# Performance work log

Hardware: AMD Instinct MI355X
Metric: run time of the kernel (lower is better)

The kernel has to match this reference:

```python
import jax, jax.numpy as jnp
import numpy as np

B, S, H, KV, D, HID = 1, 2048, 32, 8, 128, 4096
SCALE = D ** -0.5
EPS = 1e-5
QMAX = 127.0  # 8-bit symmetric fake quant


def fake_quant(x):
    # per-tensor symmetric int8 fake quantization with straight-through estimator
    s = jnp.maximum(jnp.max(jnp.abs(x)), 1e-5) / QMAX
    q = jnp.clip(jnp.round(x / s), -QMAX - 1.0, QMAX) * s
    return x + jax.lax.stop_gradient(q - x)


def rms_norm(x, w):
    xf = x.astype(jnp.float32)
    var = jnp.mean(xf * xf, axis=-1, keepdims=True)
    return (xf * jax.lax.rsqrt(var + EPS)).astype(x.dtype) * w


def rotate_half(x):
    h = x.shape[-1] // 2
    return jnp.concatenate([-x[..., h:], x[..., :h]], axis=-1)


def qlinear(x, W):
    # QuantLinear: fake-quant activation and weight, then matmul (no bias)
    return fake_quant(x) @ fake_quant(W).T


def setup_inputs() -> dict:
    key = jax.random.key(0)
    ks = jax.random.split(key, 5)
    hidden_states = jax.random.normal(ks[0], (B, S, HID), jnp.float32)
    # RoPE tables
    inv_freq = 1.0 / (10000.0 ** (np.arange(0, D, 2, dtype=np.float32) / D))
    freqs = np.outer(np.arange(S, dtype=np.float32), inv_freq)  # [S, D/2]
    emb = np.concatenate([freqs, freqs], axis=-1)  # [S, D]
    cos = jnp.asarray(np.cos(emb))[None]  # [1,S,D]
    sin = jnp.asarray(np.sin(emb))[None]
    # causal additive mask [1,1,S,S]
    mask = jnp.where(np.tril(np.ones((S, S), dtype=bool)), 0.0, -1e9).astype(jnp.float32)[None, None]
    Wq = jax.random.normal(ks[1], (H * D, HID), jnp.float32) * 0.02
    Wk = jax.random.normal(ks[2], (KV * D, HID), jnp.float32) * 0.02
    Wv = jax.random.normal(ks[3], (KV * D, HID), jnp.float32) * 0.02
    Wo = jax.random.normal(ks[4], (HID, H * D), jnp.float32) * 0.02
    q_norm_w = jnp.ones((D,), jnp.float32)
    k_norm_w = jnp.ones((D,), jnp.float32)
    return dict(hidden_states=hidden_states, cos=cos, sin=sin, attention_mask=mask,
                Wq=Wq, Wk=Wk, Wv=Wv, Wo=Wo, q_norm_w=q_norm_w, k_norm_w=k_norm_w)


def reference(hidden_states, cos, sin, attention_mask, Wq, Wk, Wv, Wo, q_norm_w, k_norm_w):
    b, s, _ = hidden_states.shape
    q = qlinear(hidden_states, Wq).reshape(b, s, H, D).transpose(0, 2, 1, 3)   # [B,H,S,D]
    k = qlinear(hidden_states, Wk).reshape(b, s, KV, D).transpose(0, 2, 1, 3)  # [B,KV,S,D]
    v = qlinear(hidden_states, Wv).reshape(b, s, KV, D).transpose(0, 2, 1, 3)
    q = rms_norm(q, q_norm_w)
    k = rms_norm(k, k_norm_w)
    c = cos[:, None]  # unsqueeze head dim -> [1,1,S,D]
    sn = sin[:, None]
    q = q * c + rotate_half(q) * sn
    k = k * c + rotate_half(k) * sn
    n_rep = H // KV
    k = jnp.repeat(k, n_rep, axis=1)  # [B,H,S,D]
    v = jnp.repeat(v, n_rep, axis=1)
    # fake-quant around QK^T
    q = fake_quant(q)
    k = fake_quant(k)
    scores = jnp.einsum('bhqd,bhkd->bhqk', q, k) * SCALE + attention_mask
    p = jax.nn.softmax(scores.astype(jnp.float32), axis=-1).astype(q.dtype)
    # fake-quant around PV
    p = fake_quant(p)
    v = fake_quant(v)
    out = jnp.einsum('bhqk,bhkd->bhqd', p, v)
    out = out.transpose(0, 2, 1, 3).reshape(b, s, H * D)
    return qlinear(out, Wo)
```

## Files before the change

kernel.cpp:

```cpp
#include <hip/hip_runtime.h>
#include <hip/hip_bf16.h>
#include <math.h>
#include <stdint.h>

#define S_LEN 2048
#define NH    32
#define NKV   8
#define HD    128
#define HIDD  4096

typedef unsigned short u16;
typedef __attribute__((ext_vector_type(4))) int i32x4;

#define GLD16(g, l) __builtin_amdgcn_global_load_lds( \
    (const __attribute__((address_space(1))) void*)(g), \
    (__attribute__((address_space(3))) void*)(l), 16, 0, 0)


__device__ __forceinline__ float slot_scale(const unsigned* slot) {
    return fmaxf(__uint_as_float(*slot), 1e-5f) / 127.0f;
}

__device__ __forceinline__ float exp2_fast(float x) {
    float r; asm("v_exp_f32 %0, %1" : "=v"(r) : "v"(x)); return r;
}
__device__ __forceinline__ float log2_fast(float x) {
    float r; asm("v_log_f32 %0, %1" : "=v"(r) : "v"(x)); return r;
}

__device__ __forceinline__ int qint(float x, float s) {
    float q = rintf(x / s);
    q = fminf(fmaxf(q, -128.0f), 127.0f);
    return (int)q;
}

__device__ __forceinline__ void block_amax_atomic(float m, unsigned* slot) {
    __shared__ float wmax[8];
    const int lane = threadIdx.x & 63;
    const int wid  = threadIdx.x >> 6;
    const int nw   = blockDim.x >> 6;
    #pragma unroll
    for (int o = 32; o; o >>= 1) m = fmaxf(m, __shfl_xor(m, o));
    if (lane == 0) wmax[wid] = m;
    __syncthreads();
    if (threadIdx.x == 0) {
        float bm = wmax[0];
        for (int i = 1; i < nw; ++i) bm = fmaxf(bm, wmax[i]);
        atomicMax(slot, __float_as_uint(bm));
    }
}

struct Amax5Args { const float* p[5]; size_t n4[5]; };
__global__ __launch_bounds__(256) void absmax5_kernel(Amax5Args a, unsigned* slots) {
    const int t = blockIdx.y;
    const float4* x4 = (const float4*)a.p[t];
    const size_t n4 = a.n4[t];
    size_t i = (size_t)blockIdx.x * blockDim.x + threadIdx.x;
    size_t stride = (size_t)gridDim.x * blockDim.x;
    float m = 0.0f;
    for (; i < n4; i += stride) {
        float4 v = x4[i];
        m = fmaxf(m, fmaxf(fmaxf(fabsf(v.x), fabsf(v.y)), fmaxf(fabsf(v.z), fabsf(v.w))));
    }
    block_amax_atomic(m, slots + t);
}

struct Quant5Args { const float* p[5]; char* o[5]; size_t n4[5]; };
__global__ __launch_bounds__(256) void quant5_kernel(Quant5Args a, const unsigned* slots) {
    const int t = blockIdx.y;
    float s = slot_scale(slots + t);
    const float4* x4 = (const float4*)a.p[t];
    unsigned* o4 = (unsigned*)a.o[t];
    const size_t n4 = a.n4[t];
    size_t i = (size_t)blockIdx.x * blockDim.x + threadIdx.x;
    size_t stride = (size_t)gridDim.x * blockDim.x;
    for (; i < n4; i += stride) {
        float4 v = x4[i];
        unsigned o = (unsigned)(qint(v.x, s) & 255)
                   | ((unsigned)(qint(v.y, s) & 255) << 8)
                   | ((unsigned)(qint(v.z, s) & 255) << 16)
                   | ((unsigned)(qint(v.w, s) & 255) << 24);
        o4[i] = o;
    }
}

__global__ __launch_bounds__(256) void quant_kernel(const float* __restrict__ x,
                                                    size_t n4, const unsigned* slot,
                                                    char* __restrict__ out) {
    float s = slot_scale(slot);
    size_t i = (size_t)blockIdx.x * blockDim.x + threadIdx.x;
    size_t stride = (size_t)gridDim.x * blockDim.x;
    const float4* x4 = (const float4*)x;
    unsigned* o4 = (unsigned*)out;
    for (; i < n4; i += stride) {
        float4 v = x4[i];
        unsigned o = (unsigned)(qint(v.x, s) & 255)
                   | ((unsigned)(qint(v.y, s) & 255) << 8)
                   | ((unsigned)(qint(v.z, s) & 255) << 16)
                   | ((unsigned)(qint(v.w, s) & 255) << 24);
        o4[i] = o;
    }
}

__device__ __forceinline__ void gemm_body(const char* __restrict__ A,
                                          const char* __restrict__ B,
                                          float* __restrict__ C,
                                          int m0, int n0, int N, int K,
                                          float scale,
                                          char* Asm, char* Bsm) {
    const int tid  = threadIdx.x;
    const int lane = tid & 63;
    const int wave = tid >> 6;
    const int wr = (wave >> 1) * 64;
    const int wc = (wave & 1) * 64;
    const int l15 = lane & 15;
    const int l4  = lane >> 4;
    const int cx  = (l4 ^ (l15 & 3)) * 16;
    const int r0  = tid >> 2;
    const int sc  = ((tid & 3) ^ ((tid >> 2) & 3)) * 16;

    i32x4 acc[4][4];
    #pragma unroll
    for (int i = 0; i < 4; ++i)
        #pragma unroll
        for (int j = 0; j < 4; ++j) acc[i][j] = (i32x4){0, 0, 0, 0};

    auto STAGE = [&](int buf, int k0) {
        GLD16(&A[(size_t)(m0 + r0) * K + k0 + sc],      &Asm[buf * 8192 + wave * 1024]);
        GLD16(&A[(size_t)(m0 + 64 + r0) * K + k0 + sc], &Asm[buf * 8192 + 4096 + wave * 1024]);
        GLD16(&B[(size_t)(n0 + r0) * K + k0 + sc],      &Bsm[buf * 8192 + wave * 1024]);
        GLD16(&B[(size_t)(n0 + 64 + r0) * K + k0 + sc], &Bsm[buf * 8192 + 4096 + wave * 1024]);
    };

    const int NT = K >> 6;
    STAGE(0, 0);
    STAGE(1, 64);
    int cur = 0;
    for (int t = 0; t < NT; ++t) {
        if (t + 1 < NT) {
            asm volatile("s_waitcnt vmcnt(4)" ::: "memory");
        } else {
            asm volatile("s_waitcnt vmcnt(0)" ::: "memory");
        }
        __builtin_amdgcn_sched_barrier(0);
        __builtin_amdgcn_s_barrier();
        __builtin_amdgcn_sched_barrier(0);
        if (t + 2 < NT) {
            int nb = cur + 2; if (nb >= 3) nb -= 3;
            STAGE(nb, (t + 2) << 6);
        }
        i32x4 af[4], bfr[4];
        #pragma unroll
        for (int i = 0; i < 4; ++i)
            af[i] = *(const i32x4*)&Asm[cur * 8192 + (wr + i * 16 + l15) * 64 + cx];
        #pragma unroll
        for (int j = 0; j < 4; ++j)
            bfr[j] = *(const i32x4*)&Bsm[cur * 8192 + (wc + j * 16 + l15) * 64 + cx];
        #pragma unroll
        for (int i = 0; i < 4; ++i)
            #pragma unroll
            for (int j = 0; j < 4; ++j)
                acc[i][j] = __builtin_amdgcn_mfma_i32_16x16x64_i8(af[i], bfr[j], acc[i][j], 0, 0, 0);
        cur += 1; if (cur == 3) cur = 0;
    }

    #pragma unroll
    for (int i = 0; i < 4; ++i)
        #pragma unroll
        for (int j = 0; j < 4; ++j)
            #pragma unroll
            for (int r = 0; r < 4; ++r) {
                int row = m0 + wr + i * 16 + l4 * 4 + r;
                int col = n0 + wc + j * 16 + l15;
                C[(size_t)row * N + col] = (float)acc[i][j][r] * scale;
            }
}

__global__ __launch_bounds__(256) void gemm_qkv_kernel(const char* __restrict__ Aq,
                                                       const char* __restrict__ Wqq,
                                                       const char* __restrict__ Wkq,
                                                       const char* __restrict__ Wvq,
                                                       float* __restrict__ qf,
                                                       float* __restrict__ kf,
                                                       float* __restrict__ vf,
                                                       const float* __restrict__ cosb,
                                                       const float* __restrict__ sinb,
                                                       const float* __restrict__ qnw,
                                                       const float* __restrict__ knw,
                                                       unsigned* __restrict__ slots) {
    __shared__ __align__(16) char Asm[3 * 8192];
    __shared__ __align__(16) char Bsm[3 * 8192];
    const int tid  = threadIdx.x;
    const int lane = tid & 63;
    const int wave = tid >> 6;
    const int l15 = lane & 15;
    const int l4  = lane >> 4;
    const int cx  = (l4 ^ (l15 & 3)) * 16;
    const int r0  = tid >> 2;
    const int sc  = ((tid & 3) ^ ((tid >> 2) & 3)) * 16;
    const int wr  = wave * 32;

    int bid = blockIdx.x;
    int swz = (bid & 7) * 96 + (bid >> 3);
    int x = swz & 15, y = swz >> 4;
    const char* B; float* C; int N, nb, kind; const unsigned* sB; const float* w;
    if (y < 32)      { B = Wqq; C = qf; N = NH * HD;  nb = y;      sB = slots + 1; kind = 0; w = qnw; }
    else if (y < 40) { B = Wkq; C = kf; N = NKV * HD; nb = y - 32; sB = slots + 2; kind = 1; w = knw; }
    else             { B = Wvq; C = vf; N = NKV * HD; nb = y - 40; sB = slots + 3; kind = 2; w = nullptr; }
    const float scale = slot_scale(slots + 0) * slot_scale(sB);
    const int m0 = x * 128, n0 = nb * 128;

    i32x4 acc[2][8];
    #pragma unroll
    for (int i = 0; i < 2; ++i)
        #pragma unroll
        for (int j = 0; j < 8; ++j) acc[i][j] = (i32x4){0, 0, 0, 0};

    auto STAGE = [&](int buf, int k0) {
        GLD16(&Aq[(size_t)(m0 + r0) * HIDD + k0 + sc],     &Asm[buf * 8192 + wave * 1024]);
        GLD16(&Aq[(size_t)(m0 + 64 + r0) * HIDD + k0 + sc],&Asm[buf * 8192 + 4096 + wave * 1024]);
        GLD16(&B[(size_t)(n0 + r0) * HIDD + k0 + sc],      &Bsm[buf * 8192 + wave * 1024]);
        GLD16(&B[(size_t)(n0 + 64 + r0) * HIDD + k0 + sc], &Bsm[buf * 8192 + 4096 + wave * 1024]);
    };

    const int NT = HIDD >> 6;
    STAGE(0, 0);
    STAGE(1, 64);
    int cur = 0;
    for (int t = 0; t < NT; ++t) {
        if (t + 1 < NT) {
            asm volatile("s_waitcnt vmcnt(4)" ::: "memory");
        } else {
            asm volatile("s_waitcnt vmcnt(0)" ::: "memory");
        }
        __builtin_amdgcn_sched_barrier(0);
        __builtin_amdgcn_s_barrier();
        __builtin_amdgcn_sched_barrier(0);
        if (t + 2 < NT) {
            int nb3 = cur + 2; if (nb3 >= 3) nb3 -= 3;
            STAGE(nb3, (t + 2) << 6);
        }
        i32x4 af[2], bfr[8];
        #pragma unroll
        for (int i = 0; i < 2; ++i)
            af[i] = *(const i32x4*)&Asm[cur * 8192 + (wr + i * 16 + l15) * 64 + cx];
        #pragma unroll
        for (int j = 0; j < 8; ++j)
            bfr[j] = *(const i32x4*)&Bsm[cur * 8192 + (j * 16 + l15) * 64 + cx];
        #pragma unroll
        for (int i = 0; i < 2; ++i)
            #pragma unroll
            for (int j = 0; j < 8; ++j)
                acc[i][j] = __builtin_amdgcn_mfma_i32_16x16x64_i8(af[i], bfr[j], acc[i][j], 0, 0, 0);
        cur += 1; if (cur == 3) cur = 0;
    }

    float lm = 0.0f;
    if (kind == 2) {
        #pragma unroll
        for (int i = 0; i < 2; ++i)
            #pragma unroll
            for (int r = 0; r < 4; ++r) {
                int row = m0 + wr + i * 16 + l4 * 4 + r;
                #pragma unroll
                for (int j = 0; j < 8; ++j) {
                    float v = (float)acc[i][j][r] * scale;
                    C[(size_t)row * N + n0 + j * 16 + l15] = v;
                    lm = fmaxf(lm, fabsf(v));
                }
            }
        __syncthreads();
        block_amax_atomic(lm, slots + 7);
    } else {
        float wj[8];
        #pragma unroll
        for (int j = 0; j < 8; ++j) wj[j] = w[j * 16 + l15];
        #pragma unroll
        for (int i = 0; i < 2; ++i)
            #pragma unroll
            for (int r = 0; r < 4; ++r) {
                int row = m0 + wr + i * 16 + l4 * 4 + r;
                float v[8];
                float ss = 0.0f;
                #pragma unroll
                for (int j = 0; j < 8; ++j) {
                    v[j] = (float)acc[i][j][r] * scale;
                    ss += v[j] * v[j];
                }
                ss += __shfl_xor(ss, 1);
                ss += __shfl_xor(ss, 2);
                ss += __shfl_xor(ss, 4);
                ss += __shfl_xor(ss, 8);
                float inv = 1.0f / sqrtf(ss * (1.0f / 128.0f) + 1e-5f);
                const float* cr = cosb + (size_t)row * 128;
                const float* sr = sinb + (size_t)row * 128;
                float yv[8];
                #pragma unroll
                for (int j = 0; j < 8; ++j) yv[j] = v[j] * inv * wj[j];
                #pragma unroll
                for (int j = 0; j < 8; ++j) {
                    int col = j * 16 + l15;
                    float o = (j < 4) ? yv[j] * cr[col] - yv[j + 4] * sr[col]
                                      : yv[j] * cr[col] + yv[j - 4] * sr[col];
                    C[(size_t)row * N + n0 + col] = o;
                    lm = fmaxf(lm, fabsf(o));
                }
            }
        __syncthreads();
        block_amax_atomic(lm, slots + (kind == 0 ? 5 : 6));
    }
}

__global__ __launch_bounds__(256) void gemm_o_kernel(const char* __restrict__ A,
                                                     const char* __restrict__ Woq,
                                                     float* __restrict__ C,
                                                     const unsigned* __restrict__ slots) {
    __shared__ __align__(16) char Asm[3 * 8192];
    __shared__ __align__(16) char Bsm[3 * 8192];
    int bid = blockIdx.x;
    int swz = (bid & 7) * 64 + (bid >> 3);
    int x = swz & 15, y = swz >> 4;
    float scale = slot_scale(slots + 8) * slot_scale(slots + 4);
    gemm_body(A, Woq, C, x * 128, y * 128, NH * HD, HIDD, scale, Asm, Bsm);
}

__global__ __launch_bounds__(256) void quant_qkv_kernel(const float* __restrict__ qx,
                                                        const float* __restrict__ kx,
                                                        const float* __restrict__ vx,
                                                        const unsigned* slots,
                                                        char* __restrict__ qq,
                                                        char* __restrict__ kq,
                                                        char* __restrict__ vtq) {
    const int bx = blockIdx.x;
    if (bx < 1024) {
        __shared__ unsigned char t8[64][36];
        const float s = slot_scale(slots + 7);
        const int t   = threadIdx.x;
        const int kvh = bx >> 7;
        const int rem = bx & 127;
        const int d0  = (rem & 3) * 32;
        const int sp0 = (rem >> 2) * 64;
        const int dl = t & 31;
        const int sb = t >> 5;
        #pragma unroll
        for (int j = 0; j < 8; ++j) {
            int spl = sb + j * 8;
            float v = vx[((size_t)(sp0 + spl) * NKV + kvh) * 128 + d0 + dl];
            t8[spl][dl] = (unsigned char)qint(v, s);
        }
        __syncthreads();
        const int dd = t >> 3;
        const int ch = t & 7;
        unsigned lo = 0, hi = 0;
        #pragma unroll
        for (int j = 0; j < 4; ++j) lo |= (unsigned)t8[ch * 8 + j][dd] << (8 * j);
        #pragma unroll
        for (int j = 0; j < 4; ++j) hi |= (unsigned)t8[ch * 8 + 4 + j][dd] << (8 * j);
        *(uint2*)&vtq[((size_t)kvh * 128 + d0 + dd) * S_LEN + sp0 + ch * 8] = make_uint2(lo, hi);
        return;
    }
    int tid = (bx - 1024) * 256 + threadIdx.x;
    const int qtot4 = S_LEN * NH * HD / 4;
    if (tid < qtot4) {
        float s = slot_scale(slots + 5);
        int e = tid * 4;
        int d  = e & 127;
        int h  = (e >> 7) & 31;
        int sp = e >> 12;
        float4 v = *(const float4*)&qx[e];
        uchar4 o;
        o.x = (unsigned char)qint(v.x, s); o.y = (unsigned char)qint(v.y, s);
        o.z = (unsigned char)qint(v.z, s); o.w = (unsigned char)qint(v.w, s);
        *(uchar4*)&qq[((size_t)h * S_LEN + sp) * 128 + d] = o;
    } else {
        tid -= qtot4;
        float s = slot_scale(slots + 6);
        int e = tid * 4;
        int d  = e & 127;
        int h  = (e >> 7) & 7;
        int sp = e >> 10;
        float4 v = *(const float4*)&kx[e];
        uchar4 o;
        o.x = (unsigned char)qint(v.x, s); o.y = (unsigned char)qint(v.y, s);
        o.z = (unsigned char)qint(v.z, s); o.w = (unsigned char)qint(v.w, s);
        *(uchar4*)&kq[((size_t)h * S_LEN + sp) * 128 + d] = o;
    }
}

__global__ __launch_bounds__(512) void attn_kernel(const char* __restrict__ Qq,
                                                   const char* __restrict__ Kq,
                                                   const char* __restrict__ Vt,
                                                   const unsigned* sq_slot,
                                                   const unsigned* sk_slot,
                                                   const unsigned* sv_slot,
                                                   float* __restrict__ O,
                                                   unsigned* amax_slot) {
    __shared__ __align__(16) char Klds[64 * 144];
    __shared__ __align__(16) char Vlds[128 * 80];
    __shared__ __align__(16) char plds[8][16 * 80];

    const int tid  = threadIdx.x;
    const int lane = tid & 63;
    const int wave = tid >> 6;
    const int mw   = wave & 3;
    const int h  = blockIdx.y;
    const int kv = h >> 2;
    const int l15 = lane & 15;
    const int l4  = lane >> 4;
    const size_t kvS = (size_t)kv * S_LEN;

    const int qtS = blockIdx.x;
    const int qtB = 31 - qtS;
    const int my_qt = (wave < 4) ? qtB : qtS;
    const int qr0 = my_qt * 64 + mw * 16;

    const float sq = slot_scale(sq_slot);
    const float sk = slot_scale(sk_slot);
    const float sv = slot_scale(sv_slot);
    const float qs2 = sq * sk * 0.08838834764831845f * 1.4426950408889634f;
    const float osc = (1.0f / 127.0f) * sv;
    const float NEG = -1e30f;

    const int krow = tid >> 3, kcol = (tid & 7) * 16;
    const int vrow = tid >> 2, vcol = (tid & 3) * 16;

    i32x4 qf2[2];
    {
        const char* qp = Qq + ((size_t)h * S_LEN + qr0 + l15) * 128 + l4 * 16;
        qf2[0] = *(const i32x4*)(qp);
        qf2[1] = *(const i32x4*)(qp + 64);
    }

    auto qk_block = [&](int hb) -> i32x4 {
        i32x4 sacc = {0, 0, 0, 0};
        #pragma unroll
        for (int c = 0; c < 2; ++c) {
            i32x4 kfa = *(const i32x4*)&Klds[(hb * 16 + l15) * 144 + c * 64 + l4 * 16];
            sacc = __builtin_amdgcn_mfma_i32_16x16x64_i8(kfa, qf2[c], sacc, 0, 0, 0);
        }
        return sacc;
    };

    float m_l = NEG, l_l = 0.0f;

    auto p1_interior = [&](int hb) {
        i32x4 sacc = qk_block(hb);
        float x0 = (float)sacc[0] * qs2, x1 = (float)sacc[1] * qs2;
        float x2 = (float)sacc[2] * qs2, x3 = (float)sacc[3] * qs2;
        float bm = fmaxf(fmaxf(x0, x1), fmaxf(x2, x3));
        float mn = fmaxf(m_l, bm);
        float ps = exp2_fast(x0 - mn) + exp2_fast(x1 - mn)
                 + exp2_fast(x2 - mn) + exp2_fast(x3 - mn);
        l_l = l_l * exp2_fast(m_l - mn) + ps;
        m_l = mn;
    };
    auto p1_diag = [&](int hb) {
        i32x4 sacc = qk_block(hb);
        float x[4];
        #pragma unroll
        for (int r = 0; r < 4; ++r) {
            float v = (float)sacc[r] * qs2;
            x[r] = ((l4 * 4 + r) > l15) ? NEG : v;
        }
        float bm = fmaxf(fmaxf(x[0], x[1]), fmaxf(x[2], x[3]));
        float mn = fmaxf(m_l, bm);
        float ps = exp2_fast(x[0] - mn) + exp2_fast(x[1] - mn)
                 + exp2_fast(x[2] - mn) + exp2_fast(x[3] - mn);
        l_l = l_l * exp2_fast(m_l - mn) + ps;
        m_l = mn;
    };

    i32x4 kreg = *(const i32x4*)&Kq[(kvS + krow) * 128 + kcol];
    #pragma unroll 1
    for (int kc = 0; kc <= qtB; ++kc) {
        __syncthreads();
        *(i32x4*)&Klds[krow * 144 + kcol] = kreg;
        __syncthreads();
        if (kc < qtB)
            kreg = *(const i32x4*)&Kq[(kvS + (kc + 1) * 64 + krow) * 128 + kcol];
        if (kc < my_qt) {
            p1_interior(0); p1_interior(1); p1_interior(2); p1_interior(3);
        } else if (kc == my_qt) {
            #pragma unroll
            for (int hb = 0; hb < 4; ++hb) {
                if (hb < mw) p1_interior(hb);
                else if (hb == mw) p1_diag(hb);
            }
        }
    }
    float cmy;
    {
        float m2 = fmaxf(m_l, __shfl_xor(m_l, 16));
        float mfin = fmaxf(m2, __shfl_xor(m2, 32));
        float t = l_l * exp2_fast(m_l - mfin);
        t += __shfl_xor(t, 16);
        t += __shfl_xor(t, 32);
        cmy = mfin - log2_fast(127.0f / t);
    }

    i32x4 oacc[8];
    #pragma unroll
    for (int dt = 0; dt < 8; ++dt) oacc[dt] = (i32x4){0, 0, 0, 0};

    auto p2_interior = [&](int hb) -> unsigned {
        i32x4 sacc = qk_block(hb);
        unsigned pack = 0;
        #pragma unroll
        for (int r = 0; r < 4; ++r) {
            float pq = rintf(exp2_fast(fmaf((float)sacc[r], qs2, -cmy)));
            pack |= ((unsigned)(int)pq) << (8 * r);
        }
        return pack;
    };
    auto p2_diag = [&](int hb) -> unsigned {
        i32x4 sacc = qk_block(hb);
        unsigned pack = 0;
        #pragma unroll
        for (int r = 0; r < 4; ++r) {
            float p = exp2_fast(fmaf((float)sacc[r], qs2, -cmy));
            float pq = ((l4 * 4 + r) > l15) ? 0.0f : rintf(p);
            pack |= ((unsigned)(int)pq) << (8 * r);
        }
        return pack;
    };
    auto pv8 = [&]() {
        i32x4 pf = *(const i32x4*)&plds[wave][l15 * 80 + l4 * 16];
        __builtin_amdgcn_s_setprio(1);
        #pragma unroll
        for (int dt = 0; dt < 8; ++dt) {
            i32x4 vfb = *(const i32x4*)&Vlds[(dt * 16 + l15) * 80 + l4 * 16];
            oacc[dt] = __builtin_amdgcn_mfma_i32_16x16x64_i8(pf, vfb, oacc[dt], 0, 0, 0);
        }
        __builtin_amdgcn_s_setprio(0);
    };

    kreg = *(const i32x4*)&Kq[(kvS + krow) * 128 + kcol];
    i32x4 vreg = *(const i32x4*)&Vt[((size_t)kv * 128 + vrow) * S_LEN + vcol];
    #pragma unroll 1
    for (int kc = 0; kc <= qtB; ++kc) {
        __syncthreads();
        *(i32x4*)&Klds[krow * 144 + kcol] = kreg;
        *(i32x4*)&Vlds[vrow * 80 + vcol] = vreg;
        __syncthreads();
        if (kc < qtB) {
            kreg = *(const i32x4*)&Kq[(kvS + (kc + 1) * 64 + krow) * 128 + kcol];
            vreg = *(const i32x4*)&Vt[((size_t)kv * 128 + vrow) * S_LEN + (kc + 1) * 64 + vcol];
        }
        if (kc < my_qt) {
            #pragma unroll
            for (int hb = 0; hb < 4; ++hb)
                *(unsigned*)&plds[wave][l15 * 80 + hb * 16 + l4 * 4] = p2_interior(hb);
            pv8();
        } else if (kc == my_qt) {
            #pragma unroll
            for (int hb = 0; hb < 4; ++hb) {
                unsigned pack = 0;
                if (hb < mw) pack = p2_interior(hb);
                else if (hb == mw) pack = p2_diag(hb);
                *(unsigned*)&plds[wave][l15 * 80 + hb * 16 + l4 * 4] = pack;
            }
            pv8();
        }
    }

    float lm = 0.0f;
    #pragma unroll
    for (int dt = 0; dt < 8; ++dt)
        #pragma unroll
        for (int r = 0; r < 4; ++r) {
            float v = (float)oacc[dt][r] * osc;
            O[(size_t)(qr0 + l4 * 4 + r) * (NH * 128) + h * 128 + dt * 16 + l15] = v;
            lm = fmaxf(lm, fabsf(v));
        }
    block_amax_atomic(lm, amax_slot);
}

extern "C" void kernel_launch(void* const* d_in, const int* in_sizes, int n_in,
                              void* d_out, int out_size, void* d_ws, size_t ws_size,
                              hipStream_t stream) {
    const float* hs   = (const float*)d_in[0];
    const float* cosb = (const float*)d_in[1];
    const float* sinb = (const float*)d_in[2];
    const float* Wq   = (const float*)d_in[4];
    const float* Wk   = (const float*)d_in[5];
    const float* Wv   = (const float*)d_in[6];
    const float* Wo   = (const float*)d_in[7];
    const float* qnw  = (const float*)d_in[8];
    const float* knw  = (const float*)d_in[9];
    float* out = (float*)d_out;

    char* ws = (char*)d_ws;
    unsigned* slots = (unsigned*)ws;
    size_t off = 256;
    auto take = [&](size_t bytes) { size_t o = off; off += (bytes + 255) & ~(size_t)255; return o; };
    char*  hsq  = (char*)(ws + take((size_t)S_LEN * HIDD));
    char*  Wqq  = (char*)(ws + take((size_t)NH * HD * HIDD));
    char*  Wkq  = (char*)(ws + take((size_t)NKV * HD * HIDD));
    char*  Wvq  = (char*)(ws + take((size_t)NKV * HD * HIDD));
    char*  Woq  = (char*)(ws + take((size_t)HIDD * NH * HD));
    float* qf   = (float*)(ws + take((size_t)S_LEN * NH * HD * 4));
    float* kf   = (float*)(ws + take((size_t)S_LEN * NKV * HD * 4));
    float* vf   = (float*)(ws + take((size_t)S_LEN * NKV * HD * 4));
    char*  qq   = (char*)(ws + take((size_t)NH * S_LEN * HD));
    char*  kq   = (char*)(ws + take((size_t)NKV * S_LEN * HD));
    char*  vtq  = (char*)(ws + take((size_t)NKV * HD * S_LEN));
    float* attnf = qf;
    char*  attnq = hsq;

    hipMemsetAsync(ws, 0, 64, stream);

    const size_t n_hs = (size_t)S_LEN * HIDD;
    const size_t n_wq = (size_t)NH * HD * HIDD;
    const size_t n_wk = (size_t)NKV * HD * HIDD;

    Amax5Args aa;
    aa.p[0] = hs; aa.p[1] = Wq; aa.p[2] = Wk; aa.p[3] = Wv; aa.p[4] = Wo;
    aa.n4[0] = n_hs / 4; aa.n4[1] = n_wq / 4; aa.n4[2] = n_wk / 4;
    aa.n4[3] = n_wk / 4; aa.n4[4] = n_wq / 4;
    absmax5_kernel<<<dim3(512, 5), 256, 0, stream>>>(aa, slots);

    Quant5Args qa;
    qa.p[0] = hs; qa.p[1] = Wq; qa.p[2] = Wk; qa.p[3] = Wv; qa.p[4] = Wo;
    qa.o[0] = hsq; qa.o[1] = Wqq; qa.o[2] = Wkq; qa.o[3] = Wvq; qa.o[4] = Woq;
    qa.n4[0] = n_hs / 4; qa.n4[1] = n_wq / 4; qa.n4[2] = n_wk / 4;
    qa.n4[3] = n_wk / 4; qa.n4[4] = n_wq / 4;
    quant5_kernel<<<dim3(1024, 5), 256, 0, stream>>>(qa, slots);

    gemm_qkv_kernel<<<768, 256, 0, stream>>>(hsq, Wqq, Wkq, Wvq, qf, kf, vf,
                                             cosb, sinb, qnw, knw, slots);

    quant_qkv_kernel<<<1024 + 10240, 256, 0, stream>>>(qf, kf, vf, slots, qq, kq, vtq);

    attn_kernel<<<dim3(16, NH), 512, 0, stream>>>(qq, kq, vtq,
                                                  slots + 5, slots + 6, slots + 7,
                                                  attnf, slots + 8);

    quant_kernel<<<2048, 256, 0, stream>>>(attnf, n_hs / 4, slots + 8, attnq);
    gemm_o_kernel<<<512, 256, 0, stream>>>(attnq, Woq, out, slots);
    (void)in_sizes; (void)n_in; (void)out_size; (void)ws_size;
}
```

Baseline: 343.5 us.

## Retile QKV GEMM waves into a 2x2 grid with cross-wave RMS reduction

Changes each wave's tile from 32x128 to 64x64, with column groups chosen so that RoPE's rotate-half partners stay in the same wave. The aim is to cut LDS fragment loads per MFMA: each step now loads 8 fragments instead of 10. Because a head's 128 columns now span two waves, the RMS-norm sum of squares is exchanged through a small shared buffer, which adds an extra __syncthreads in the epilogue.

```diff
diff --git a/kernel.cpp b/kernel.cpp
--- a/kernel.cpp
+++ b/kernel.cpp
@@ -190,15 +190,20 @@
                                                        unsigned* __restrict__ slots) {
     __shared__ __align__(16) char Asm[3 * 8192];
     __shared__ __align__(16) char Bsm[3 * 8192];
+    __shared__ float sstmp[128][2];
     const int tid  = threadIdx.x;
     const int lane = tid & 63;
     const int wave = tid >> 6;
+    const int wr = (wave >> 1) * 64;
+    const int wh = wave & 1;
     const int l15 = lane & 15;
     const int l4  = lane >> 4;
     const int cx  = (l4 ^ (l15 & 3)) * 16;
     const int r0  = tid >> 2;
     const int sc  = ((tid & 3) ^ ((tid >> 2) & 3)) * 16;
-    const int wr  = wave * 32;
+    int cb[4];
+    #pragma unroll
+    for (int j = 0; j < 4; ++j) cb[j] = wh * 32 + (j & 1) * 16 + (j >> 1) * 64;
 
     int bid = blockIdx.x;
     int swz = (bid & 7) * 96 + (bid >> 3);
@@ -210,17 +215,17 @@
     const float scale = slot_scale(slots + 0) * slot_scale(sB);
     const int m0 = x * 128, n0 = nb * 128;
 
-    i32x4 acc[2][8];
+    i32x4 acc[4][4];
     #pragma unroll
-    for (int i = 0; i < 2; ++i)
-        #pragma unroll
-        for (int j = 0; j < 8; ++j) acc[i][j] = (i32x4){0, 0, 0, 0};
+    for (int i = 0; i < 4; ++i)
+        #pragma unroll
+        for (int j = 0; j < 4; ++j) acc[i][j] = (i32x4){0, 0, 0, 0};
 
     auto STAGE = [&](int buf, int k0) {
-        GLD16(&Aq[(size_t)(m0 + r0) * HIDD + k0 + sc],     &Asm[buf * 8192 + wave * 1024]);
-        GLD16(&Aq[(size_t)(m0 + 64 + r0) * HIDD + k0 + sc],&Asm[buf * 8192 + 4096 + wave * 1024]);
-        GLD16(&B[(size_t)(n0 + r0) * HIDD + k0 + sc],      &Bsm[buf * 8192 + wave * 1024]);
-        GLD16(&B[(size_t)(n0 + 64 + r0) * HIDD + k0 + sc], &Bsm[buf * 8192 + 4096 + wave * 1024]);
+        GLD16(&Aq[(size_t)(m0 + r0) * HIDD + k0 + sc],      &Asm[buf * 8192 + wave * 1024]);
+        GLD16(&Aq[(size_t)(m0 + 64 + r0) * HIDD + k0 + sc], &Asm[buf * 8192 + 4096 + wave * 1024]);
+        GLD16(&B[(size_t)(n0 + r0) * HIDD + k0 + sc],       &Bsm[buf * 8192 + wave * 1024]);
+        GLD16(&B[(size_t)(n0 + 64 + r0) * HIDD + k0 + sc],  &Bsm[buf * 8192 + 4096 + wave * 1024]);
     };
 
     const int NT = HIDD >> 6;
@@ -240,17 +245,17 @@
             int nb3 = cur + 2; if (nb3 >= 3) nb3 -= 3;
             STAGE(nb3, (t + 2) << 6);
         }
-        i32x4 af[2], bfr[8];
-        #pragma unroll
-        for (int i = 0; i < 2; ++i)
+        i32x4 af[4], bfr[4];
+        #pragma unroll
+        for (int i = 0; i < 4; ++i)
             af[i] = *(const i32x4*)&Asm[cur * 8192 + (wr + i * 16 + l15) * 64 + cx];
         #pragma unroll
-        for (int j = 0; j < 8; ++j)
-            bfr[j] = *(const i32x4*)&Bsm[cur * 8192 + (j * 16 + l15) * 64 + cx];
-        #pragma unroll
-        for (int i = 0; i < 2; ++i)
-            #pragma unroll
-            for (int j = 0; j < 8; ++j)
+        for (int j = 0; j < 4; ++j)
+            bfr[j] = *(const i32x4*)&Bsm[cur * 8192 + (cb[j] + l15) * 64 + cx];
+        #pragma unroll
+        for (int i = 0; i < 4; ++i)
+            #pragma unroll
+            for (int j = 0; j < 4; ++j)
                 acc[i][j] = __builtin_amdgcn_mfma_i32_16x16x64_i8(af[i], bfr[j], acc[i][j], 0, 0, 0);
         cur += 1; if (cur == 3) cur = 0;
     }
@@ -258,50 +263,58 @@
     float lm = 0.0f;
     if (kind == 2) {
         #pragma unroll
-        for (int i = 0; i < 2; ++i)
+        for (int i = 0; i < 4; ++i)
             #pragma unroll
             for (int r = 0; r < 4; ++r) {
                 int row = m0 + wr + i * 16 + l4 * 4 + r;
                 #pragma unroll
-                for (int j = 0; j < 8; ++j) {
+                for (int j = 0; j < 4; ++j) {
                     float v = (float)acc[i][j][r] * scale;
-                    C[(size_t)row * N + n0 + j * 16 + l15] = v;
+                    C[(size_t)row * N + n0 + cb[j] + l15] = v;
                     lm = fmaxf(lm, fabsf(v));
                 }
             }
         __syncthreads();
         block_amax_atomic(lm, slots + 7);
     } else {
-        float wj[8];
-        #pragma unroll
-        for (int j = 0; j < 8; ++j) wj[j] = w[j * 16 + l15];
-        #pragma unroll
-        for (int i = 0; i < 2; ++i)
+        #pragma unroll
+        for (int i = 0; i < 4; ++i)
             #pragma unroll
             for (int r = 0; r < 4; ++r) {
-                int row = m0 + wr + i * 16 + l4 * 4 + r;
-                float v[8];
                 float ss = 0.0f;
                 #pragma unroll
-                for (int j = 0; j < 8; ++j) {
-                    v[j] = (float)acc[i][j][r] * scale;
-                    ss += v[j] * v[j];
+                for (int j = 0; j < 4; ++j) {
+                    float v = (float)acc[i][j][r] * scale;
+                    ss += v * v;
                 }
                 ss += __shfl_xor(ss, 1);
                 ss += __shfl_xor(ss, 2);
                 ss += __shfl_xor(ss, 4);
                 ss += __shfl_xor(ss, 8);
+                if (l15 == 0) sstmp[wr + i * 16 + l4 * 4 + r][wh] = ss;
+            }
+        __syncthreads();
+        float wj[4];
+        #pragma unroll
+        for (int j = 0; j < 4; ++j) wj[j] = w[cb[j] + l15];
+        #pragma unroll
+        for (int i = 0; i < 4; ++i)
+            #pragma unroll
+            for (int r = 0; r < 4; ++r) {
+                int rloc = wr + i * 16 + l4 * 4 + r;
+                int row  = m0 + rloc;
+                float ss = sstmp[rloc][0] + sstmp[rloc][1];
                 float inv = 1.0f / sqrtf(ss * (1.0f / 128.0f) + 1e-5f);
                 const float* cr = cosb + (size_t)row * 128;
                 const float* sr = sinb + (size_t)row * 128;
-                float yv[8];
+                float yv[4];
                 #pragma unroll
-                for (int j = 0; j < 8; ++j) yv[j] = v[j] * inv * wj[j];
+                for (int j = 0; j < 4; ++j) yv[j] = (float)acc[i][j][r] * scale * inv * wj[j];
                 #pragma unroll
-                for (int j = 0; j < 8; ++j) {
-                    int col = j * 16 + l15;
-                    float o = (j < 4) ? yv[j] * cr[col] - yv[j + 4] * sr[col]
-                                      : yv[j] * cr[col] + yv[j - 4] * sr[col];
+                for (int j = 0; j < 4; ++j) {
+                    int col = cb[j] + l15;
+                    float o = (j < 2) ? yv[j] * cr[col] - yv[j + 2] * sr[col]
+                                      : yv[j] * cr[col] + yv[j - 2] * sr[col];
                     C[(size_t)row * N + n0 + col] = o;
                     lm = fmaxf(lm, fabsf(o));
                 }
```

New measurement: 352.3 us. 1.03x slower.
